# Kernel optimization log

Hardware: AMD Instinct MI355X
Metric: run time of the kernel (lower is better)

## Reference

```python
import jax, jax.numpy as jnp
import numpy as np

B, N, C_IN, C_OUT, CHEB_K, EMB = 32, 2048, 128, 128, 3, 128
LN_EPS = 1e-12


def setup_inputs() -> dict:
    key = jax.random.key(0)
    k0, k1, k2, k3 = jax.random.split(key, 4)
    return {
        "x": jax.random.normal(k0, (B, N, C_IN), dtype=jnp.float32),
        "node_embeddings": jax.random.normal(k1, (N, EMB), dtype=jnp.float32),
        "weights_pool": jax.random.normal(k2, (EMB, CHEB_K, C_IN, C_OUT), dtype=jnp.float32) * 0.02,
        "bias_pool": jax.random.normal(k3, (EMB, C_OUT), dtype=jnp.float32) * 0.02,
        "ln_gamma": jnp.ones((EMB,), dtype=jnp.float32),
        "ln_beta": jnp.zeros((EMB,), dtype=jnp.float32),
    }


def reference(x, node_embeddings, weights_pool, bias_pool, ln_gamma, ln_beta):
    # x: [B, N, C_in]; node_embeddings: [N, D]
    cheb_k = weights_pool.shape[1]
    n = node_embeddings.shape[0]

    # LayerNorm over embed dim (biased variance, eps=1e-12); dropout is eval-mode identity
    mu = jnp.mean(node_embeddings, axis=-1, keepdims=True)
    var = jnp.mean(jnp.square(node_embeddings - mu), axis=-1, keepdims=True)
    e = (node_embeddings - mu) * jax.lax.rsqrt(var + LN_EPS) * ln_gamma + ln_beta

    # Adaptive adjacency: softmax(elu(E E^T)) over last dim (mask=None path)
    supports = jax.nn.softmax(jax.nn.elu(e @ e.T), axis=-1)  # [N, N]

    # Chebyshev polynomial set: T0=I, T1=A, Tk = 2A Tk-1 - Tk-2
    s_list = [jnp.eye(n, dtype=x.dtype), supports]
    for _ in range(2, cheb_k):
        s_list.append(2.0 * supports @ s_list[-1] - s_list[-2])
    S = jnp.stack(s_list, axis=0)  # [K, N, N]

    # Hypernetwork: per-node weights and bias
    weights = jnp.einsum("nd,dkio->nkio", e, weights_pool)  # [N, K, C_in, C_out]
    bias = e @ bias_pool  # [N, C_out]

    # Graph conv: gather neighborhoods per Chebyshev order, then per-node GEMM
    x_g = jnp.einsum("knm,bmc->bnkc", S, x)  # [B, N, K, C_in]
    out = jnp.einsum("bnki,nkio->bno", x_g, weights) + bias  # [B, N, C_out]
    return out
```

## Files before the change

kernel.cpp:

```cpp
#include <hip/hip_runtime.h>

#define DI __device__ __forceinline__

typedef unsigned short u16;
typedef short short8 __attribute__((ext_vector_type(8)));
typedef float f32x4 __attribute__((ext_vector_type(4)));
typedef u16 u16x4 __attribute__((ext_vector_type(4)));

#define NN 2048
#define CC 128
#define BB 32
#define DD 128
#define OO 128
#define KI 384
#define JJ 49152

DI u16 f2bf(float f) {
  union { float f; unsigned u; } v; v.f = f;
  return (u16)((v.u + 0x7fffu + ((v.u >> 16) & 1u)) >> 16);
}

typedef __attribute__((address_space(3))) unsigned int lds_u32;
typedef __attribute__((address_space(1))) unsigned int glob_u32;

DI void gl16(const void* g, void* l) {
  __builtin_amdgcn_global_load_lds((const glob_u32*)g, (lds_u32*)l, 16, 0, 0);
}

__global__ __launch_bounds__(128)
void k_ln(const float* __restrict__ emb, const float* __restrict__ gam,
          const float* __restrict__ bet, float* __restrict__ e, u16* __restrict__ ebf) {
  __shared__ float s2[2], q2[2];
  const int n = blockIdx.x, t = threadIdx.x;
  const float v = emb[(size_t)n * DD + t];
  float s = v;
  #pragma unroll
  for (int off = 32; off; off >>= 1) s += __shfl_down(s, off);
  if ((t & 63) == 0) s2[t >> 6] = s;
  __syncthreads();
  const float mu = (s2[0] + s2[1]) * (1.f / 128.f);
  const float dv = v - mu;
  float q = dv * dv;
  #pragma unroll
  for (int off = 32; off; off >>= 1) q += __shfl_down(q, off);
  if ((t & 63) == 0) q2[t >> 6] = q;
  __syncthreads();
  const float var = (q2[0] + q2[1]) * (1.f / 128.f);
  const float ev = dv * rsqrtf(var + 1e-12f) * gam[t] + bet[t];
  e[(size_t)n * DD + t] = ev;
  ebf[(size_t)n * DD + t] = f2bf(ev);
}

__global__ __launch_bounds__(256)
void k_score(const float* __restrict__ e, u16* __restrict__ Abf) {
  __shared__ float en[8 * 128];
  __shared__ float red[4][8];
  const int t = threadIdx.x, w = t >> 6;
  const int nb = blockIdx.x * 8;
  for (int i = t; i < 1024; i += 256) en[i] = e[(size_t)nb * DD + i];
  __syncthreads();
  const int m0 = t * 8;
  float a[8][8];
  #pragma unroll
  for (int mj = 0; mj < 8; ++mj)
    #pragma unroll
    for (int nn2 = 0; nn2 < 8; ++nn2) a[mj][nn2] = 0.f;
  for (int d = 0; d < 128; d += 4) {
    float enb[8][4];
    #pragma unroll
    for (int nn2 = 0; nn2 < 8; ++nn2) {
      const float4 ev = *(const float4*)&en[nn2 * 128 + d];
      enb[nn2][0] = ev.x; enb[nn2][1] = ev.y; enb[nn2][2] = ev.z; enb[nn2][3] = ev.w;
    }
    #pragma unroll
    for (int mj = 0; mj < 8; ++mj) {
      const float4 v = *(const float4*)&e[(size_t)(m0 + mj) * DD + d];
      #pragma unroll
      for (int nn2 = 0; nn2 < 8; ++nn2)
        a[mj][nn2] += v.x * enb[nn2][0] + v.y * enb[nn2][1] + v.z * enb[nn2][2] + v.w * enb[nn2][3];
    }
  }
  #pragma unroll
  for (int mj = 0; mj < 8; ++mj)
    #pragma unroll
    for (int nn2 = 0; nn2 < 8; ++nn2) {
      const float s = a[mj][nn2];
      a[mj][nn2] = (s > 0.f) ? s : expm1f(s);
    }
  float mx[8];
  #pragma unroll
  for (int nn2 = 0; nn2 < 8; ++nn2) {
    float m_ = a[0][nn2];
    #pragma unroll
    for (int mj = 1; mj < 8; ++mj) m_ = fmaxf(m_, a[mj][nn2]);
    #pragma unroll
    for (int off = 32; off; off >>= 1) m_ = fmaxf(m_, __shfl_xor(m_, off));
    mx[nn2] = m_;
  }
  if ((t & 63) == 0) {
    #pragma unroll
    for (int nn2 = 0; nn2 < 8; ++nn2) red[w][nn2] = mx[nn2];
  }
  __syncthreads();
  #pragma unroll
  for (int nn2 = 0; nn2 < 8; ++nn2)
    mx[nn2] = fmaxf(fmaxf(red[0][nn2], red[1][nn2]), fmaxf(red[2][nn2], red[3][nn2]));
  __syncthreads();
  float sm[8];
  #pragma unroll
  for (int nn2 = 0; nn2 < 8; ++nn2) sm[nn2] = 0.f;
  #pragma unroll
  for (int mj = 0; mj < 8; ++mj)
    #pragma unroll
    for (int nn2 = 0; nn2 < 8; ++nn2) {
      a[mj][nn2] = expf(a[mj][nn2] - mx[nn2]);
      sm[nn2] += a[mj][nn2];
    }
  #pragma unroll
  for (int nn2 = 0; nn2 < 8; ++nn2) {
    #pragma unroll
    for (int off = 32; off; off >>= 1) sm[nn2] += __shfl_xor(sm[nn2], off);
  }
  if ((t & 63) == 0) {
    #pragma unroll
    for (int nn2 = 0; nn2 < 8; ++nn2) red[w][nn2] = sm[nn2];
  }
  __syncthreads();
  #pragma unroll
  for (int nn2 = 0; nn2 < 8; ++nn2) {
    const float tot = red[0][nn2] + red[1][nn2] + red[2][nn2] + red[3][nn2];
    const float inv = 1.f / tot;
    short8 pk;
    #pragma unroll
    for (int mj = 0; mj < 8; ++mj) pk[mj] = (short)f2bf(a[mj][nn2] * inv);
    *(short8*)(Abf + (size_t)(nb + nn2) * NN + m0) = pk;
  }
}

__global__ __launch_bounds__(256)
void k_tc(const float* __restrict__ x, u16* __restrict__ xt) {
  __shared__ float ld[64 * 68];
  const int t = threadIdx.x;
  const int m0 = blockIdx.x * 64, c0 = blockIdx.y * 64, b = blockIdx.z;
  const float* xb = x + (size_t)b * NN * CC;
  #pragma unroll
  for (int i = 0; i < 4; ++i) {
    const int m = i * 16 + (t >> 4), c4 = (t & 15) * 4;
    *(float4*)&ld[m * 68 + c4] = *(const float4*)&xb[(size_t)(m0 + m) * CC + c0 + c4];
  }
  __syncthreads();
  u16* xtb = xt + (size_t)b * CC * NN;
  #pragma unroll
  for (int i = 0; i < 4; ++i) {
    const int c = i * 16 + (t >> 4), m4 = (t & 15) * 4;
    u16x4 v = { f2bf(ld[(m4 + 0) * 68 + c]), f2bf(ld[(m4 + 1) * 68 + c]),
                f2bf(ld[(m4 + 2) * 68 + c]), f2bf(ld[(m4 + 3) * 68 + c]) };
    *(u16x4*)&xtb[(size_t)(c0 + c) * NN + m0 + m4] = v;
  }
}

__global__ __launch_bounds__(256)
void k_wpt(const float* __restrict__ wp, u16* __restrict__ wpt) {
  __shared__ float ld[64 * 68];
  const int t = threadIdx.x;
  const int d0 = blockIdx.x * 64, o0 = blockIdx.y * 64, ki = blockIdx.z;
  #pragma unroll
  for (int i = 0; i < 4; ++i) {
    const int d = i * 16 + (t >> 4), o4 = (t & 15) * 4;
    *(float4*)&ld[d * 68 + o4] = *(const float4*)&wp[((size_t)(d0 + d) * KI + ki) * OO + o0 + o4];
  }
  __syncthreads();
  #pragma unroll
  for (int i = 0; i < 4; ++i) {
    const int o = i * 16 + (t >> 4), d4 = (t & 15) * 4;
    u16x4 v = { f2bf(ld[(d4 + 0) * 68 + o]), f2bf(ld[(d4 + 1) * 68 + o]),
                f2bf(ld[(d4 + 2) * 68 + o]), f2bf(ld[(d4 + 3) * 68 + o]) };
    *(u16x4*)&wpt[((size_t)(o0 + o) * KI + ki) * DD + d0 + d4] = v;
  }
}

__global__ __launch_bounds__(128)
void k_bias(const float* __restrict__ e, const float* __restrict__ bp, float* __restrict__ bias) {
  const int n = blockIdx.x, o = threadIdx.x;
  const float* er = e + (size_t)n * DD;
  float acc = 0.f;
  for (int d = 0; d < 128; ++d) acc = fmaf(er[d], bp[(size_t)d * OO + o], acc);
  bias[(size_t)n * OO + o] = acc;
}

template<int MODE>
__global__ __launch_bounds__(256, 2)
void gemm_bf16(const u16* __restrict__ Ab, int lda,
               const u16* __restrict__ Bb, int ldb, int ksteps,
               u16* __restrict__ out0, u16* __restrict__ out1,
               const float* __restrict__ xaux) {
  __shared__ char smem[34816];
  const int t = threadIdx.x;
  const int w = t >> 6, l = t & 63;
  const int l15 = l & 15, kg = l >> 4;
  const int wr = (w >> 1) * 64, wc = (w & 1) * 64;

  const u16 *Abase, *Bbase;
  int row0 = 0, col0 = 0, b = 0;
  if constexpr (MODE == 0) {
    row0 = blockIdx.x * 128; b = blockIdx.y;
    Abase = Ab + (size_t)row0 * lda;
    Bbase = Bb + (size_t)b * CC * NN;
  } else if constexpr (MODE == 1) {
    col0 = blockIdx.x * 128; b = blockIdx.y;
    Abase = Ab + (size_t)b * CC * NN;
    Bbase = Bb + (size_t)col0 * NN;
  } else {
    row0 = blockIdx.x * 128; col0 = blockIdx.y * 128;
    Abase = Ab + (size_t)row0 * 128;
    Bbase = Bb + (size_t)col0 * 128;
  }

  f32x4 acc[4][4];
  #pragma unroll
  for (int i = 0; i < 4; ++i)
    #pragma unroll
    for (int j = 0; j < 4; ++j) { f32x4 z = {0.f, 0.f, 0.f, 0.f}; acc[i][j] = z; }

  const int ra = t >> 3, sa = t & 7;
  for (int kt = 0; kt < ksteps; ++kt) {
    const int k0 = kt * 64;
    __syncthreads();
    #pragma unroll
    for (int i = 0; i < 4; ++i) {
      const int r = i * 32 + ra;
      const int ss = sa ^ (r & 7);
      gl16(Abase + (size_t)r * lda + k0 + ss * 8, smem + i * 4096 + t * 16);
    }
    #pragma unroll
    for (int i = 0; i < 4; ++i) {
      const int r = i * 32 + ra;
      const int ss = sa ^ (r & 7);
      gl16(Bbase + (size_t)r * ldb + k0 + ss * 8, smem + 16384 + i * 4096 + t * 16);
    }
    __syncthreads();
    short8 af[2][4], bfv[2][4];
    #pragma unroll
    for (int mt = 0; mt < 4; ++mt) {
      const int row = wr + mt * 16 + l15;
      #pragma unroll
      for (int ks = 0; ks < 2; ++ks) {
        const int sl = (ks * 4 + kg) ^ (row & 7);
        af[ks][mt] = *(const short8*)(smem + row * 128 + sl * 16);
      }
    }
    #pragma unroll
    for (int nt = 0; nt < 4; ++nt) {
      const int row = wc + nt * 16 + l15;
      #pragma unroll
      for (int ks = 0; ks < 2; ++ks) {
        const int sl = (ks * 4 + kg) ^ (row & 7);
        bfv[ks][nt] = *(const short8*)(smem + 16384 + row * 128 + sl * 16);
      }
    }
    #pragma unroll
    for (int ks = 0; ks < 2; ++ks)
      #pragma unroll
      for (int mt = 0; mt < 4; ++mt)
        #pragma unroll
        for (int nt = 0; nt < 4; ++nt)
          acc[mt][nt] = __builtin_amdgcn_mfma_f32_16x16x32_bf16(af[ks][mt], bfv[ks][nt], acc[mt][nt], 0, 0, 0);
  }

  if constexpr (MODE == 0) {
    u16* y1t = out0 + (size_t)b * CC * NN;
    #pragma unroll
    for (int mt = 0; mt < 4; ++mt) {
      const int n_ = row0 + wr + mt * 16 + kg * 4;
      #pragma unroll
      for (int nt = 0; nt < 4; ++nt) {
        const int c_ = wc + nt * 16 + l15;
        u16x4 v = { f2bf(acc[mt][nt][0]), f2bf(acc[mt][nt][1]),
                    f2bf(acc[mt][nt][2]), f2bf(acc[mt][nt][3]) };
        *(u16x4*)(y1t + (size_t)c_ * NN + n_) = v;
      }
    }
    __syncthreads();
    u16* L = (u16*)smem;
    #pragma unroll
    for (int mt = 0; mt < 4; ++mt) {
      const int nl = wr + mt * 16 + kg * 4;
      #pragma unroll
      for (int nt = 0; nt < 4; ++nt) {
        const int c_ = wc + nt * 16 + l15;
        #pragma unroll
        for (int r = 0; r < 4; ++r) L[(nl + r) * 136 + c_] = f2bf(acc[mt][nt][r]);
      }
    }
    __syncthreads();
    u16* y1o = out1 + (size_t)b * NN * CC;
    const int nl2 = t >> 1, ch = (t & 1) * 64;
    #pragma unroll
    for (int q = 0; q < 8; ++q) {
      short8 vv = *(const short8*)(L + nl2 * 136 + ch + q * 8);
      *(short8*)(y1o + (size_t)(row0 + nl2) * CC + ch + q * 8) = vv;
    }
  } else if constexpr (MODE == 1) {
    const float* xb = xaux + (size_t)b * NN * CC;
    u16* y2b = out0 + (size_t)b * NN * CC;
    #pragma unroll
    for (int mt = 0; mt < 4; ++mt) {
      const int c_ = wr + mt * 16 + kg * 4;
      #pragma unroll
      for (int nt = 0; nt < 4; ++nt) {
        const int n_ = col0 + wc + nt * 16 + l15;
        const float4 xv = *(const float4*)(xb + (size_t)n_ * CC + c_);
        u16x4 v = { f2bf(2.f * acc[mt][nt][0] - xv.x), f2bf(2.f * acc[mt][nt][1] - xv.y),
                    f2bf(2.f * acc[mt][nt][2] - xv.z), f2bf(2.f * acc[mt][nt][3] - xv.w) };
        *(u16x4*)(y2b + (size_t)n_ * CC + c_) = v;
      }
    }
  } else {
    u16* wtb = out0 + (size_t)col0 * JJ;
    #pragma unroll
    for (int mt = 0; mt < 4; ++mt) {
      const int j_ = row0 + wr + mt * 16 + kg * 4;
      #pragma unroll
      for (int nt = 0; nt < 4; ++nt) {
        const int nl = wc + nt * 16 + l15;
        u16x4 v = { f2bf(acc[mt][nt][0]), f2bf(acc[mt][nt][1]),
                    f2bf(acc[mt][nt][2]), f2bf(acc[mt][nt][3]) };
        *(u16x4*)(wtb + (size_t)nl * JJ + j_) = v;
      }
    }
  }
}

__global__ __launch_bounds__(256, 4)
void stage_b(const float* __restrict__ x, const u16* __restrict__ y1,
             const u16* __restrict__ y2, const u16* __restrict__ Wt,
             const float* __restrict__ bias, float* __restrict__ out, int nbase) {
  const int t = threadIdx.x, w = t >> 6, l = t & 63;
  const int l15 = l & 15, kg = l >> 4;
  const int n = nbase + blockIdx.x;
  const u16* Wn = Wt + (size_t)blockIdx.x * JJ;
  f32x4 acc[2][2];
  {
    f32x4 z = {0.f, 0.f, 0.f, 0.f};
    acc[0][0] = z; acc[0][1] = z; acc[1][0] = z; acc[1][1] = z;
  }
  #pragma unroll
  for (int ch2 = 0; ch2 < 3; ++ch2) {
    #pragma unroll
    for (int ks = 0; ks < 4; ++ks) {
      short8 af[2];
      #pragma unroll
      for (int mt = 0; mt < 2; ++mt) {
        const int bb2 = mt * 16 + l15;
        const size_t base = ((size_t)bb2 * NN + n) * CC + ks * 32 + kg * 8;
        if (ch2 == 0) {
          float4 v0 = *(const float4*)(x + base);
          float4 v1 = *(const float4*)(x + base + 4);
          short8 s;
          s[0] = (short)f2bf(v0.x); s[1] = (short)f2bf(v0.y);
          s[2] = (short)f2bf(v0.z); s[3] = (short)f2bf(v0.w);
          s[4] = (short)f2bf(v1.x); s[5] = (short)f2bf(v1.y);
          s[6] = (short)f2bf(v1.z); s[7] = (short)f2bf(v1.w);
          af[mt] = s;
        } else {
          const u16* src = (ch2 == 1) ? y1 : y2;
          af[mt] = *(const short8*)(src + base);
        }
      }
      #pragma unroll
      for (int ot = 0; ot < 2; ++ot) {
        const int o = w * 32 + ot * 16 + l15;
        const int ki = ch2 * 128 + ks * 32 + kg * 8;
        short8 bv = *(const short8*)(Wn + (size_t)o * KI + ki);
        acc[0][ot] = __builtin_amdgcn_mfma_f32_16x16x32_bf16(af[0], bv, acc[0][ot], 0, 0, 0);
        acc[1][ot] = __builtin_amdgcn_mfma_f32_16x16x32_bf16(af[1], bv, acc[1][ot], 0, 0, 0);
      }
    }
  }
  #pragma unroll
  for (int ot = 0; ot < 2; ++ot) {
    const int o = w * 32 + ot * 16 + l15;
    const float bs = bias[(size_t)n * OO + o];
    #pragma unroll
    for (int mt = 0; mt < 2; ++mt)
      #pragma unroll
      for (int r = 0; r < 4; ++r) {
        const int bb2 = mt * 16 + kg * 4 + r;
        out[((size_t)bb2 * NN + n) * OO + o] = acc[mt][ot][r] + bs;
      }
  }
}

extern "C" void kernel_launch(void* const* d_in, const int* in_sizes, int n_in,
                              void* d_out, int out_size, void* d_ws, size_t ws_size,
                              hipStream_t stream) {
  (void)in_sizes; (void)n_in; (void)out_size;
  const float* x   = (const float*)d_in[0];
  const float* emb = (const float*)d_in[1];
  const float* wp  = (const float*)d_in[2];
  const float* bp  = (const float*)d_in[3];
  const float* gam = (const float*)d_in[4];
  const float* bet = (const float*)d_in[5];
  float* out = (float*)d_out;
  char* ws = (char*)d_ws;

  size_t off = 0;
  auto alloc = [&](size_t bytes) -> void* {
    void* p = (void*)(ws + off);
    off += (bytes + 511) & ~(size_t)511;
    return p;
  };
  float* e    = (float*)alloc((size_t)NN * DD * 4);
  u16*   ebf  = (u16*)  alloc((size_t)NN * DD * 2);
  float* bias = (float*)alloc((size_t)NN * OO * 4);
  u16*   Abf  = (u16*)  alloc((size_t)NN * NN * 2);
  u16*   xt   = (u16*)  alloc((size_t)BB * CC * NN * 2);
  u16*   y1t  = (u16*)  alloc((size_t)BB * CC * NN * 2);
  u16*   y1   = (u16*)  alloc((size_t)BB * NN * CC * 2);
  u16*   y2   = (u16*)  alloc((size_t)BB * NN * CC * 2);
  u16*   wpt  = (u16*)  alloc((size_t)JJ * DD * 2);
  const size_t rem = (ws_size > off) ? (ws_size - off) : 0;
  int chunk = 1024;
  while (chunk > 128 && (size_t)chunk * JJ * 2 > rem) chunk >>= 1;
  u16* wt = (u16*)alloc((size_t)chunk * JJ * 2);

  k_ln<<<NN, 128, 0, stream>>>(emb, gam, bet, e, ebf);
  k_score<<<NN / 8, 256, 0, stream>>>(e, Abf);
  k_tc<<<dim3(NN / 64, CC / 64, BB), 256, 0, stream>>>(x, xt);
  k_wpt<<<dim3(2, 2, KI), 256, 0, stream>>>(wp, wpt);
  k_bias<<<NN, 128, 0, stream>>>(e, bp, bias);

  gemm_bf16<0><<<dim3(16, 32), 256, 0, stream>>>(Abf, NN, xt, NN, 32, y1t, y1, nullptr);
  gemm_bf16<1><<<dim3(16, 32), 256, 0, stream>>>(y1t, NN, Abf, NN, 32, y2, nullptr, x);

  for (int nb = 0; nb < NN; nb += chunk) {
    gemm_bf16<2><<<dim3(JJ / 128, chunk / 128), 256, 0, stream>>>(
        wpt, DD, ebf + (size_t)nb * DD, DD, 2, wt, nullptr, nullptr);
    stage_b<<<chunk, 256, 0, stream>>>(x, y1, y2, wt, bias, out, nb);
  }
}
```

Before: 425.4 us.

## Compute adjacency scores with split-bf16 MFMA GEMM and pre-convert x to bf16

Replaces the FP32 scalar score kernel with an MFMA GEMM that approximates E·E^T from hi/lo bf16 splits (three product terms), writes ELU'd scores to a scratch buffer aliased onto the weight workspace, and then applies the row softmax in a separate kernel. The transpose kernel also emits a bf16 copy of x so stage_b loads bf16 directly and no longer converts fp32 in its inner loop. The hypernetwork chunk size drops from 1024 to 512. This adds an extra full N×N fp32 round trip and twice as many chunk launches in exchange for tensor-core score computation.

Measured after the change: 388.2 us. -8.7%, faster.

```diff
diff --git a/kernel.cpp b/kernel.cpp
--- a/kernel.cpp
+++ b/kernel.cpp
@@ -19,6 +19,10 @@
   union { float f; unsigned u; } v; v.f = f;
   return (u16)((v.u + 0x7fffu + ((v.u >> 16) & 1u)) >> 16);
 }
+DI float bf2f(u16 h) {
+  union { unsigned u; float f; } v; v.u = ((unsigned)h) << 16;
+  return v.f;
+}
 
 typedef __attribute__((address_space(3))) unsigned int lds_u32;
 typedef __attribute__((address_space(1))) unsigned int glob_u32;
@@ -29,7 +33,8 @@
 
 __global__ __launch_bounds__(128)
 void k_ln(const float* __restrict__ emb, const float* __restrict__ gam,
-          const float* __restrict__ bet, float* __restrict__ e, u16* __restrict__ ebf) {
+          const float* __restrict__ bet, float* __restrict__ e,
+          u16* __restrict__ ehi, u16* __restrict__ elo) {
   __shared__ float s2[2], q2[2];
   const int n = blockIdx.x, t = threadIdx.x;
   const float v = emb[(size_t)n * DD + t];
@@ -48,105 +53,129 @@
   const float var = (q2[0] + q2[1]) * (1.f / 128.f);
   const float ev = dv * rsqrtf(var + 1e-12f) * gam[t] + bet[t];
   e[(size_t)n * DD + t] = ev;
-  ebf[(size_t)n * DD + t] = f2bf(ev);
+  const u16 hi = f2bf(ev);
+  ehi[(size_t)n * DD + t] = hi;
+  elo[(size_t)n * DD + t] = f2bf(ev - bf2f(hi));
+}
+
+__global__ __launch_bounds__(256, 2)
+void k_zg(const u16* __restrict__ ehi, const u16* __restrict__ elo, float* __restrict__ Z) {
+  __shared__ char smem[32768];
+  const int t = threadIdx.x;
+  const int w = t >> 6, l = t & 63;
+  const int l15 = l & 15, kg = l >> 4;
+  const int wr = (w >> 1) * 64, wc = (w & 1) * 64;
+  const int row0 = blockIdx.x * 128, col0 = blockIdx.y * 128;
+
+  f32x4 acc[4][4];
+  #pragma unroll
+  for (int i = 0; i < 4; ++i)
+    #pragma unroll
+    for (int j = 0; j < 4; ++j) { f32x4 z = {0.f, 0.f, 0.f, 0.f}; acc[i][j] = z; }
+
+  const int ra = t >> 3, sa = t & 7;
+  #pragma unroll 1
+  for (int it = 0; it < 6; ++it) {
+    const int term = it >> 1;
+    const int k0 = (it & 1) * 64;
+    const u16* As = (term == 2) ? elo : ehi;
+    const u16* Bs = (term == 1) ? elo : ehi;
+    __syncthreads();
+    #pragma unroll
+    for (int i = 0; i < 4; ++i) {
+      const int r = i * 32 + ra;
+      const int ss = sa ^ (r & 7);
+      gl16(As + (size_t)(row0 + r) * DD + k0 + ss * 8, smem + i * 4096 + t * 16);
+      gl16(Bs + (size_t)(col0 + r) * DD + k0 + ss * 8, smem + 16384 + i * 4096 + t * 16);
+    }
+    __syncthreads();
+    short8 af[2][4], bfv[2][4];
+    #pragma unroll
+    for (int mt = 0; mt < 4; ++mt) {
+      const int row = wr + mt * 16 + l15;
+      #pragma unroll
+      for (int ks = 0; ks < 2; ++ks) {
+        const int sl = (ks * 4 + kg) ^ (row & 7);
+        af[ks][mt] = *(const short8*)(smem + row * 128 + sl * 16);
+      }
+    }
+    #pragma unroll
+    for (int nt = 0; nt < 4; ++nt) {
+      const int row = wc + nt * 16 + l15;
+      #pragma unroll
+      for (int ks = 0; ks < 2; ++ks) {
+        const int sl = (ks * 4 + kg) ^ (row & 7);
+        bfv[ks][nt] = *(const short8*)(smem + 16384 + row * 128 + sl * 16);
+      }
+    }
+    #pragma unroll
+    for (int ks = 0; ks < 2; ++ks)
+      #pragma unroll
+      for (int mt = 0; mt < 4; ++mt)
+        #pragma unroll
+        for (int nt = 0; nt < 4; ++nt)
+          acc[mt][nt] = __builtin_amdgcn_mfma_f32_16x16x32_bf16(af[ks][mt], bfv[ks][nt], acc[mt][nt], 0, 0, 0);
+  }
+  #pragma unroll
+  for (int mt = 0; mt < 4; ++mt) {
+    const int n_ = row0 + wr + mt * 16 + kg * 4;
+    #pragma unroll
+    for (int nt = 0; nt < 4; ++nt) {
+      const int m_ = col0 + wc + nt * 16 + l15;
+      #pragma unroll
+      for (int r = 0; r < 4; ++r) {
+        const float v = acc[mt][nt][r];
+        Z[(size_t)(n_ + r) * NN + m_] = (v > 0.f) ? v : expm1f(v);
+      }
+    }
+  }
 }
 
 __global__ __launch_bounds__(256)
-void k_score(const float* __restrict__ e, u16* __restrict__ Abf) {
-  __shared__ float en[8 * 128];
-  __shared__ float red[4][8];
-  const int t = threadIdx.x, w = t >> 6;
-  const int nb = blockIdx.x * 8;
-  for (int i = t; i < 1024; i += 256) en[i] = e[(size_t)nb * DD + i];
-  __syncthreads();
-  const int m0 = t * 8;
-  float a[8][8];
-  #pragma unroll
-  for (int mj = 0; mj < 8; ++mj)
-    #pragma unroll
-    for (int nn2 = 0; nn2 < 8; ++nn2) a[mj][nn2] = 0.f;
-  for (int d = 0; d < 128; d += 4) {
-    float enb[8][4];
-    #pragma unroll
-    for (int nn2 = 0; nn2 < 8; ++nn2) {
-      const float4 ev = *(const float4*)&en[nn2 * 128 + d];
-      enb[nn2][0] = ev.x; enb[nn2][1] = ev.y; enb[nn2][2] = ev.z; enb[nn2][3] = ev.w;
-    }
-    #pragma unroll
-    for (int mj = 0; mj < 8; ++mj) {
-      const float4 v = *(const float4*)&e[(size_t)(m0 + mj) * DD + d];
-      #pragma unroll
-      for (int nn2 = 0; nn2 < 8; ++nn2)
-        a[mj][nn2] += v.x * enb[nn2][0] + v.y * enb[nn2][1] + v.z * enb[nn2][2] + v.w * enb[nn2][3];
-    }
-  }
-  #pragma unroll
-  for (int mj = 0; mj < 8; ++mj)
-    #pragma unroll
-    for (int nn2 = 0; nn2 < 8; ++nn2) {
-      const float s = a[mj][nn2];
-      a[mj][nn2] = (s > 0.f) ? s : expm1f(s);
-    }
-  float mx[8];
-  #pragma unroll
-  for (int nn2 = 0; nn2 < 8; ++nn2) {
-    float m_ = a[0][nn2];
-    #pragma unroll
-    for (int mj = 1; mj < 8; ++mj) m_ = fmaxf(m_, a[mj][nn2]);
-    #pragma unroll
-    for (int off = 32; off; off >>= 1) m_ = fmaxf(m_, __shfl_xor(m_, off));
-    mx[nn2] = m_;
-  }
-  if ((t & 63) == 0) {
-    #pragma unroll
-    for (int nn2 = 0; nn2 < 8; ++nn2) red[w][nn2] = mx[nn2];
-  }
-  __syncthreads();
-  #pragma unroll
-  for (int nn2 = 0; nn2 < 8; ++nn2)
-    mx[nn2] = fmaxf(fmaxf(red[0][nn2], red[1][nn2]), fmaxf(red[2][nn2], red[3][nn2]));
-  __syncthreads();
-  float sm[8];
-  #pragma unroll
-  for (int nn2 = 0; nn2 < 8; ++nn2) sm[nn2] = 0.f;
-  #pragma unroll
-  for (int mj = 0; mj < 8; ++mj)
-    #pragma unroll
-    for (int nn2 = 0; nn2 < 8; ++nn2) {
-      a[mj][nn2] = expf(a[mj][nn2] - mx[nn2]);
-      sm[nn2] += a[mj][nn2];
-    }
-  #pragma unroll
-  for (int nn2 = 0; nn2 < 8; ++nn2) {
-    #pragma unroll
-    for (int off = 32; off; off >>= 1) sm[nn2] += __shfl_xor(sm[nn2], off);
-  }
-  if ((t & 63) == 0) {
-    #pragma unroll
-    for (int nn2 = 0; nn2 < 8; ++nn2) red[w][nn2] = sm[nn2];
-  }
-  __syncthreads();
-  #pragma unroll
-  for (int nn2 = 0; nn2 < 8; ++nn2) {
-    const float tot = red[0][nn2] + red[1][nn2] + red[2][nn2] + red[3][nn2];
-    const float inv = 1.f / tot;
-    short8 pk;
-    #pragma unroll
-    for (int mj = 0; mj < 8; ++mj) pk[mj] = (short)f2bf(a[mj][nn2] * inv);
-    *(short8*)(Abf + (size_t)(nb + nn2) * NN + m0) = pk;
-  }
+void k_sm(const float* __restrict__ Z, u16* __restrict__ Abf) {
+  __shared__ float red[4];
+  const int n = blockIdx.x, t = threadIdx.x, w = t >> 6;
+  const float* zr = Z + (size_t)n * NN + t * 8;
+  float4 v0 = *(const float4*)(zr);
+  float4 v1 = *(const float4*)(zr + 4);
+  float z[8] = {v0.x, v0.y, v0.z, v0.w, v1.x, v1.y, v1.z, v1.w};
+  float mx = z[0];
+  #pragma unroll
+  for (int i = 1; i < 8; ++i) mx = fmaxf(mx, z[i]);
+  #pragma unroll
+  for (int off = 32; off; off >>= 1) mx = fmaxf(mx, __shfl_xor(mx, off));
+  if ((t & 63) == 0) red[w] = mx;
+  __syncthreads();
+  mx = fmaxf(fmaxf(red[0], red[1]), fmaxf(red[2], red[3]));
+  __syncthreads();
+  float sm = 0.f;
+  #pragma unroll
+  for (int i = 0; i < 8; ++i) { z[i] = expf(z[i] - mx); sm += z[i]; }
+  #pragma unroll
+  for (int off = 32; off; off >>= 1) sm += __shfl_xor(sm, off);
+  if ((t & 63) == 0) red[w] = sm;
+  __syncthreads();
+  const float inv = 1.f / (red[0] + red[1] + red[2] + red[3]);
+  short8 pk;
+  #pragma unroll
+  for (int i = 0; i < 8; ++i) pk[i] = (short)f2bf(z[i] * inv);
+  *(short8*)(Abf + (size_t)n * NN + t * 8) = pk;
 }
 
 __global__ __launch_bounds__(256)
-void k_tc(const float* __restrict__ x, u16* __restrict__ xt) {
+void k_tc(const float* __restrict__ x, u16* __restrict__ xt, u16* __restrict__ xbf) {
   __shared__ float ld[64 * 68];
   const int t = threadIdx.x;
   const int m0 = blockIdx.x * 64, c0 = blockIdx.y * 64, b = blockIdx.z;
   const float* xb = x + (size_t)b * NN * CC;
+  u16* xfb = xbf + (size_t)b * NN * CC;
   #pragma unroll
   for (int i = 0; i < 4; ++i) {
     const int m = i * 16 + (t >> 4), c4 = (t & 15) * 4;
-    *(float4*)&ld[m * 68 + c4] = *(const float4*)&xb[(size_t)(m0 + m) * CC + c0 + c4];
+    const float4 v = *(const float4*)&xb[(size_t)(m0 + m) * CC + c0 + c4];
+    *(float4*)&ld[m * 68 + c4] = v;
+    u16x4 cv = { f2bf(v.x), f2bf(v.y), f2bf(v.z), f2bf(v.w) };
+    *(u16x4*)&xfb[(size_t)(m0 + m) * CC + c0 + c4] = cv;
   }
   __syncthreads();
   u16* xtb = xt + (size_t)b * CC * NN;
@@ -332,7 +361,7 @@
 }
 
 __global__ __launch_bounds__(256, 4)
-void stage_b(const float* __restrict__ x, const u16* __restrict__ y1,
+void stage_b(const u16* __restrict__ xbf, const u16* __restrict__ y1,
              const u16* __restrict__ y2, const u16* __restrict__ Wt,
              const float* __restrict__ bias, float* __restrict__ out, int nbase) {
   const int t = threadIdx.x, w = t >> 6, l = t & 63;
@@ -346,26 +375,14 @@
   }
   #pragma unroll
   for (int ch2 = 0; ch2 < 3; ++ch2) {
+    const u16* src = (ch2 == 0) ? xbf : (ch2 == 1) ? y1 : y2;
     #pragma unroll
     for (int ks = 0; ks < 4; ++ks) {
       short8 af[2];
       #pragma unroll
       for (int mt = 0; mt < 2; ++mt) {
         const int bb2 = mt * 16 + l15;
-        const size_t base = ((size_t)bb2 * NN + n) * CC + ks * 32 + kg * 8;
-        if (ch2 == 0) {
-          float4 v0 = *(const float4*)(x + base);
-          float4 v1 = *(const float4*)(x + base + 4);
-          short8 s;
-          s[0] = (short)f2bf(v0.x); s[1] = (short)f2bf(v0.y);
-          s[2] = (short)f2bf(v0.z); s[3] = (short)f2bf(v0.w);
-          s[4] = (short)f2bf(v1.x); s[5] = (short)f2bf(v1.y);
-          s[6] = (short)f2bf(v1.z); s[7] = (short)f2bf(v1.w);
-          af[mt] = s;
-        } else {
-          const u16* src = (ch2 == 1) ? y1 : y2;
-          af[mt] = *(const short8*)(src + base);
-        }
+        af[mt] = *(const short8*)(src + ((size_t)bb2 * NN + n) * CC + ks * 32 + kg * 8);
       }
       #pragma unroll
       for (int ot = 0; ot < 2; ++ot) {
@@ -411,22 +428,26 @@
     return p;
   };
   float* e    = (float*)alloc((size_t)NN * DD * 4);
-  u16*   ebf  = (u16*)  alloc((size_t)NN * DD * 2);
+  u16*   ehi  = (u16*)  alloc((size_t)NN * DD * 2);
+  u16*   elo  = (u16*)  alloc((size_t)NN * DD * 2);
   float* bias = (float*)alloc((size_t)NN * OO * 4);
   u16*   Abf  = (u16*)  alloc((size_t)NN * NN * 2);
   u16*   xt   = (u16*)  alloc((size_t)BB * CC * NN * 2);
+  u16*   xbf  = (u16*)  alloc((size_t)BB * NN * CC * 2);
   u16*   y1t  = (u16*)  alloc((size_t)BB * CC * NN * 2);
   u16*   y1   = (u16*)  alloc((size_t)BB * NN * CC * 2);
   u16*   y2   = (u16*)  alloc((size_t)BB * NN * CC * 2);
   u16*   wpt  = (u16*)  alloc((size_t)JJ * DD * 2);
   const size_t rem = (ws_size > off) ? (ws_size - off) : 0;
-  int chunk = 1024;
+  int chunk = 512;
   while (chunk > 128 && (size_t)chunk * JJ * 2 > rem) chunk >>= 1;
   u16* wt = (u16*)alloc((size_t)chunk * JJ * 2);
-
-  k_ln<<<NN, 128, 0, stream>>>(emb, gam, bet, e, ebf);
-  k_score<<<NN / 8, 256, 0, stream>>>(e, Abf);
-  k_tc<<<dim3(NN / 64, CC / 64, BB), 256, 0, stream>>>(x, xt);
+  float* Z = (float*)wt;
+
+  k_ln<<<NN, 128, 0, stream>>>(emb, gam, bet, e, ehi, elo);
+  k_zg<<<dim3(16, 16), 256, 0, stream>>>(ehi, elo, Z);
+  k_sm<<<NN, 256, 0, stream>>>(Z, Abf);
+  k_tc<<<dim3(NN / 64, CC / 64, BB), 256, 0, stream>>>(x, xt, xbf);
   k_wpt<<<dim3(2, 2, KI), 256, 0, stream>>>(wp, wpt);
   k_bias<<<NN, 128, 0, stream>>>(e, bp, bias);
 
@@ -435,7 +456,7 @@
 
   for (int nb = 0; nb < NN; nb += chunk) {
     gemm_bf16<2><<<dim3(JJ / 128, chunk / 128), 256, 0, stream>>>(
-        wpt, DD, ebf + (size_t)nb * DD, DD, 2, wt, nullptr, nullptr);
-    stage_b<<<chunk, 256, 0, stream>>>(x, y1, y2, wt, bias, out, nb);
-  }
-}
+        wpt, DD, ehi + (size_t)nb * DD, DD, 2, wt, nullptr, nullptr);
+    stage_b<<<chunk, 256, 0, stream>>>(xbf, y1, y2, wt, bias, out, nb);
+  }
+}
```
